# Optimization experiments

Measured on AMD Instinct MI355X. Metric: run time of the kernel, lower is better.

Reference implementation:

```python
import jax, jax.numpy as jnp
import numpy as np

N = 8192
IN_DIM = 128
OUT_DIM = 128


def setup_inputs() -> dict:
    key = jax.random.key(0)
    k_adj, k_feat, k_w = jax.random.split(key, 3)
    raw = jax.random.uniform(k_adj, (N, N), dtype=jnp.float32)
    adj = jnp.where(raw > 0.99, jnp.float32(1.0), jnp.float32(0.0))
    features = jax.random.normal(k_feat, (N, IN_DIM), dtype=jnp.float32)
    W = jax.random.normal(k_w, (OUT_DIM, IN_DIM), dtype=jnp.float32) * (1.0 / np.sqrt(IN_DIM))
    b = jnp.zeros((OUT_DIM,), dtype=jnp.float32)
    return {"adj": adj, "features": features, "W": W, "b": b}


def reference(adj, features, W, b):
    # adj + I  (original builds a sparse identity then densifies)
    n = adj.shape[0]
    adj = adj + jnp.eye(n, dtype=adj.dtype)
    row_sum = jnp.sum(adj, axis=1)                      # [N]
    d_inv_sqrt = jnp.power(row_sum, -0.5)
    d_inv_sqrt = jnp.where(jnp.isinf(d_inv_sqrt), 0.0, d_inv_sqrt)
    # diag(d) @ adj @ diag(d) == broadcast scale rows and cols (same math)
    norm_adj = d_inv_sqrt[:, None] * adj * d_inv_sqrt[None, :]
    out = norm_adj @ features                           # [N, in_dim]
    out = out @ W.T + b                                 # linear
    return jax.nn.relu(out)
```

## Files before the change

### kernel.cpp

```cpp
#include <hip/hip_runtime.h>
#include <hip/hip_bf16.h>

#define NROWS 8192
#define DIM 128
#define CAP 192
#define WPR 128

__global__ __launch_bounds__(256) void k1_scan(const float* __restrict__ adj,
                                               unsigned* __restrict__ counts,
                                               unsigned long long* __restrict__ bm) {
    int row = blockIdx.x;
    int t = threadIdx.x, lane = t & 63, w = t >> 6;
    const float4* arow = (const float4*)(adj + (size_t)row * NROWS);
    unsigned long long* brow = bm + (size_t)row * WPR;
    __shared__ unsigned s_c[4];
    unsigned my = 0;
#pragma unroll
    for (int k = 0; k < 8; ++k) {
        float4 v = arow[k * 256 + t];
        unsigned long long m0 = __ballot(v.x != 0.f);
        unsigned long long m1 = __ballot(v.y != 0.f);
        unsigned long long m2 = __ballot(v.z != 0.f);
        unsigned long long m3 = __ballot(v.w != 0.f);
        if (lane == 0) {
            unsigned long long* p = brow + (size_t)(k * 4 + w) * 4;
            p[0] = m0; p[1] = m1; p[2] = m2; p[3] = m3;
            my += (unsigned)(__popcll(m0) + __popcll(m1) + __popcll(m2) + __popcll(m3));
        }
    }
    if (lane == 0) s_c[w] = my;
    __syncthreads();
    if (t == 0) counts[row] = s_c[0] + s_c[1] + s_c[2] + s_c[3];
}

#define K2ROWS 16
__global__ __launch_bounds__(256) void k2_gemm(const float* __restrict__ feat,
                                               const float* __restrict__ W,
                                               const unsigned* __restrict__ counts,
                                               float* __restrict__ d,
                                               __hip_bfloat16* __restrict__ h) {
    __shared__ __align__(16) float sWt[128][132];
    __shared__ __align__(16) float sF[K2ROWS][128];
    __shared__ float s_d[K2ROWS];
    int t = threadIdx.x;
    int row0 = blockIdx.x * K2ROWS;

#pragma unroll
    for (int it = 0; it < 16; ++it) {
        int f4 = it * 256 + t;
        float4 wv = ((const float4*)W)[f4];
        int c = f4 >> 5;
        int k = (f4 & 31) * 4;
        sWt[k + 0][c] = wv.x; sWt[k + 1][c] = wv.y;
        sWt[k + 2][c] = wv.z; sWt[k + 3][c] = wv.w;
    }
#pragma unroll
    for (int it = 0; it < 2; ++it) {
        int idx4 = it * 256 + t;
        float4 fv = ((const float4*)(feat + (size_t)row0 * DIM))[idx4];
        int r = idx4 >> 5;
        int k = (idx4 & 31) * 4;
        sF[r][k + 0] = fv.x; sF[r][k + 1] = fv.y;
        sF[r][k + 2] = fv.z; sF[r][k + 3] = fv.w;
    }
    if (t < K2ROWS) {
        float dv = rsqrtf((float)(counts[row0 + t] + 1u));
        s_d[t] = dv;
        d[row0 + t] = dv;
    }
    __syncthreads();

    int r2 = (t >> 5) * 2;
    int c4 = (t & 31) * 4;
    float acc[2][4] = {{0.f,0.f,0.f,0.f},{0.f,0.f,0.f,0.f}};
#pragma unroll 4
    for (int k = 0; k < 128; ++k) {
        float4 wv = *(const float4*)&sWt[k][c4];
        float f0 = sF[r2][k];
        float f1 = sF[r2 + 1][k];
        acc[0][0] = fmaf(f0, wv.x, acc[0][0]);
        acc[0][1] = fmaf(f0, wv.y, acc[0][1]);
        acc[0][2] = fmaf(f0, wv.z, acc[0][2]);
        acc[0][3] = fmaf(f0, wv.w, acc[0][3]);
        acc[1][0] = fmaf(f1, wv.x, acc[1][0]);
        acc[1][1] = fmaf(f1, wv.y, acc[1][1]);
        acc[1][2] = fmaf(f1, wv.z, acc[1][2]);
        acc[1][3] = fmaf(f1, wv.w, acc[1][3]);
    }
#pragma unroll
    for (int rr = 0; rr < 2; ++rr) {
        float dv = s_d[r2 + rr];
        size_t o = (size_t)(row0 + r2 + rr) * DIM + c4;
#pragma unroll
        for (int cc = 0; cc < 4; ++cc)
            h[o + cc] = __float2bfloat16(acc[rr][cc] * dv);
    }
}

__device__ __forceinline__ float bflo(unsigned p) { return __uint_as_float(p << 16); }
__device__ __forceinline__ float bfhi(unsigned p) { return __uint_as_float(p & 0xffff0000u); }

__global__ __launch_bounds__(256) void k3_gather(const unsigned long long* __restrict__ bm,
                                                 const unsigned* __restrict__ h32,
                                                 const float* __restrict__ d,
                                                 const float* __restrict__ b,
                                                 float* __restrict__ out) {
    __shared__ unsigned short s_idx[4][CAP];
    __shared__ unsigned s_cnt[4];
    int w = threadIdx.x >> 6, l = threadIdx.x & 63;
    int row = (blockIdx.x << 2) + w;
    if (l == 0) s_cnt[w] = 0;
    __syncthreads();

    const unsigned long long* brow = bm + (size_t)row * WPR;
    unsigned long long wd0 = brow[l];
    unsigned long long wd1 = brow[l + 64];
    unsigned pc = (unsigned)(__popcll(wd0) + __popcll(wd1));
    unsigned off = pc ? atomicAdd(&s_cnt[w], pc) : 0u;
    {
        unsigned long long m = wd0; int W = l;
        while (m && off < CAP) {
            int i = __ffsll((long long)m) - 1; m &= m - 1;
            s_idx[w][off++] = (unsigned short)(((W >> 2) << 8) | (i << 2) | (W & 3));
        }
        m = wd1; W = l + 64;
        while (m && off < CAP) {
            int i = __ffsll((long long)m) - 1; m &= m - 1;
            s_idx[w][off++] = (unsigned short)(((W >> 2) << 8) | (i << 2) | (W & 3));
        }
    }
    __syncthreads();
    unsigned cnt = s_cnt[w];
    if (cnt > CAP) cnt = CAP;

    float a0, a1;
    { unsigned p = h32[(size_t)row * 64 + l]; a0 = bflo(p); a1 = bfhi(p); }
    unsigned e = 0;
    for (; e + 4 <= cnt; e += 4) {
        int j0 = s_idx[w][e + 0];
        int j1 = s_idx[w][e + 1];
        int j2 = s_idx[w][e + 2];
        int j3 = s_idx[w][e + 3];
        unsigned p0 = h32[(size_t)j0 * 64 + l];
        unsigned p1 = h32[(size_t)j1 * 64 + l];
        unsigned p2 = h32[(size_t)j2 * 64 + l];
        unsigned p3 = h32[(size_t)j3 * 64 + l];
        a0 += bflo(p0); a1 += bfhi(p0);
        a0 += bflo(p1); a1 += bfhi(p1);
        a0 += bflo(p2); a1 += bfhi(p2);
        a0 += bflo(p3); a1 += bfhi(p3);
    }
    for (; e < cnt; ++e) {
        unsigned p = h32[(size_t)s_idx[w][e] * 64 + l];
        a0 += bflo(p); a1 += bfhi(p);
    }
    float dv = d[row];
    float2 bb = ((const float2*)b)[l];
    float o0 = fmaxf(fmaf(dv, a0, bb.x), 0.f);
    float o1 = fmaxf(fmaf(dv, a1, bb.y), 0.f);
    ((float2*)out)[(size_t)row * 64 + l] = make_float2(o0, o1);
}

extern "C" void kernel_launch(void* const* d_in, const int* in_sizes, int n_in,
                              void* d_out, int out_size, void* d_ws, size_t ws_size,
                              hipStream_t stream) {
    const float* adj  = (const float*)d_in[0];
    const float* feat = (const float*)d_in[1];
    const float* W    = (const float*)d_in[2];
    const float* b    = (const float*)d_in[3];
    float* out = (float*)d_out;

    char* ws = (char*)d_ws;
    unsigned*           counts = (unsigned*)ws;
    float*              d      = (float*)(ws + 32768);
    __hip_bfloat16*     h      = (__hip_bfloat16*)(ws + 65536);
    unsigned long long* bmask  = (unsigned long long*)(ws + 65536 + 2097152);

    k1_scan<<<NROWS, 256, 0, stream>>>(adj, counts, bmask);
    k2_gemm<<<NROWS / K2ROWS, 256, 0, stream>>>(feat, W, counts, d, h);
    k3_gather<<<NROWS / 4, 256, 0, stream>>>(bmask, (const unsigned*)h, d, b, out);
}
```

Before: 73.82 us.

## Use grid-stride adjacency scan and move degree counting into GEMM kernel

The scan kernel now runs 2048 blocks that each stride over the adjacency matrix as a flat float4 array, writing ballot masks with 16-byte stores and no longer computing per-row counts. Degree counting moves into the GEMM kernel, which popcounts each row's bitmask from the workspace with shared-memory atomics. The aim is to cut block launch overhead and reduction syncs in the bandwidth-bound 256 MB scan. The cost is an extra bitmask read and extra barriers in the GEMM kernel.

```diff
diff --git a/kernel.cpp b/kernel.cpp
--- a/kernel.cpp
+++ b/kernel.cpp
@@ -7,43 +7,48 @@
 #define WPR 128
 
 __global__ __launch_bounds__(256) void k1_scan(const float* __restrict__ adj,
-                                               unsigned* __restrict__ counts,
                                                unsigned long long* __restrict__ bm) {
-    int row = blockIdx.x;
-    int t = threadIdx.x, lane = t & 63, w = t >> 6;
-    const float4* arow = (const float4*)(adj + (size_t)row * NROWS);
-    unsigned long long* brow = bm + (size_t)row * WPR;
-    __shared__ unsigned s_c[4];
-    unsigned my = 0;
-#pragma unroll
-    for (int k = 0; k < 8; ++k) {
-        float4 v = arow[k * 256 + t];
+    const int t = threadIdx.x, lane = t & 63;
+    const float4* a4 = (const float4*)adj;
+    size_t g = (size_t)blockIdx.x * 256 + t;
+#pragma unroll 4
+    for (int it = 0; it < 32; ++it, g += 524288) {
+        float4 v = a4[g];
         unsigned long long m0 = __ballot(v.x != 0.f);
         unsigned long long m1 = __ballot(v.y != 0.f);
         unsigned long long m2 = __ballot(v.z != 0.f);
         unsigned long long m3 = __ballot(v.w != 0.f);
         if (lane == 0) {
-            unsigned long long* p = brow + (size_t)(k * 4 + w) * 4;
-            p[0] = m0; p[1] = m1; p[2] = m2; p[3] = m3;
-            my += (unsigned)(__popcll(m0) + __popcll(m1) + __popcll(m2) + __popcll(m3));
+            ulonglong2* p = (ulonglong2*)(bm + (g >> 6) * 4);
+            p[0] = make_ulonglong2(m0, m1);
+            p[1] = make_ulonglong2(m2, m3);
         }
     }
-    if (lane == 0) s_c[w] = my;
-    __syncthreads();
-    if (t == 0) counts[row] = s_c[0] + s_c[1] + s_c[2] + s_c[3];
 }
 
 #define K2ROWS 16
 __global__ __launch_bounds__(256) void k2_gemm(const float* __restrict__ feat,
                                                const float* __restrict__ W,
-                                               const unsigned* __restrict__ counts,
+                                               const unsigned long long* __restrict__ bm,
                                                float* __restrict__ d,
                                                __hip_bfloat16* __restrict__ h) {
     __shared__ __align__(16) float sWt[128][132];
     __shared__ __align__(16) float sF[K2ROWS][128];
     __shared__ float s_d[K2ROWS];
+    __shared__ unsigned s_c[K2ROWS];
     int t = threadIdx.x;
     int row0 = blockIdx.x * K2ROWS;
+
+    if (t < K2ROWS) s_c[t] = 0;
+    __syncthreads();
+
+    {
+        const unsigned long long* br = bm + (size_t)(row0 + (t >> 4)) * WPR + (size_t)(t & 15) * 8;
+        unsigned pc = 0;
+#pragma unroll
+        for (int i = 0; i < 8; ++i) pc += (unsigned)__popcll(br[i]);
+        atomicAdd(&s_c[t >> 4], pc);
+    }
 
 #pragma unroll
     for (int it = 0; it < 16; ++it) {
@@ -63,12 +68,12 @@
         sF[r][k + 0] = fv.x; sF[r][k + 1] = fv.y;
         sF[r][k + 2] = fv.z; sF[r][k + 3] = fv.w;
     }
+    __syncthreads();
     if (t < K2ROWS) {
-        float dv = rsqrtf((float)(counts[row0 + t] + 1u));
+        float dv = rsqrtf((float)(s_c[t] + 1u));
         s_d[t] = dv;
         d[row0 + t] = dv;
     }
-    __syncthreads();
 
     int r2 = (t >> 5) * 2;
     int c4 = (t & 31) * 4;
@@ -87,6 +92,7 @@
         acc[1][2] = fmaf(f1, wv.z, acc[1][2]);
         acc[1][3] = fmaf(f1, wv.w, acc[1][3]);
     }
+    __syncthreads();
 #pragma unroll
     for (int rr = 0; rr < 2; ++rr) {
         float dv = s_d[r2 + rr];
@@ -118,15 +124,15 @@
     unsigned pc = (unsigned)(__popcll(wd0) + __popcll(wd1));
     unsigned off = pc ? atomicAdd(&s_cnt[w], pc) : 0u;
     {
-        unsigned long long m = wd0; int W = l;
+        unsigned long long m = wd0; int Wd = l;
         while (m && off < CAP) {
             int i = __ffsll((long long)m) - 1; m &= m - 1;
-            s_idx[w][off++] = (unsigned short)(((W >> 2) << 8) | (i << 2) | (W & 3));
+            s_idx[w][off++] = (unsigned short)(((Wd >> 2) << 8) | (i << 2) | (Wd & 3));
         }
-        m = wd1; W = l + 64;
+        m = wd1; Wd = l + 64;
         while (m && off < CAP) {
             int i = __ffsll((long long)m) - 1; m &= m - 1;
-            s_idx[w][off++] = (unsigned short)(((W >> 2) << 8) | (i << 2) | (W & 3));
+            s_idx[w][off++] = (unsigned short)(((Wd >> 2) << 8) | (i << 2) | (Wd & 3));
         }
     }
     __syncthreads();
@@ -171,12 +177,11 @@
     float* out = (float*)d_out;
 
     char* ws = (char*)d_ws;
-    unsigned*           counts = (unsigned*)ws;
-    float*              d      = (float*)(ws + 32768);
-    __hip_bfloat16*     h      = (__hip_bfloat16*)(ws + 65536);
-    unsigned long long* bmask  = (unsigned long long*)(ws + 65536 + 2097152);
+    float*              d     = (float*)ws;
+    __hip_bfloat16*     h     = (__hip_bfloat16*)(ws + 65536);
+    unsigned long long* bmask = (unsigned long long*)(ws + 65536 + 2097152);
 
-    k1_scan<<<NROWS, 256, 0, stream>>>(adj, counts, bmask);
-    k2_gemm<<<NROWS / K2ROWS, 256, 0, stream>>>(feat, W, counts, d, h);
+    k1_scan<<<2048, 256, 0, stream>>>(adj, bmask);
+    k2_gemm<<<NROWS / K2ROWS, 256, 0, stream>>>(feat, W, bmask, d, h);
     k3_gather<<<NROWS / 4, 256, 0, stream>>>(bmask, (const unsigned*)h, d, b, out);
 }
```

Result: slower. 79.61 us (+7.8%).
